# Kernel tuning notes

Measured on AMD Instinct MI355X. Metric: run time of the kernel, lower is better.

The kernel has to match this reference:

```python
import jax, jax.numpy as jnp
import numpy as np

EMBED_DIM = 1024
B, S = 4, 2048

def setup_inputs() -> dict:
    key = jax.random.key(0)
    ks = jax.random.split(key, 9)
    D = EMBED_DIM
    scale = 1.0 / np.sqrt(D)
    scale2 = 1.0 / np.sqrt(2 * D)
    return {
        "classical_state": jax.random.normal(ks[0], (B, S, D), jnp.float32),
        "quantum_state": jax.random.normal(ks[1], (B, S, D), jnp.float32),
        "Wc": jax.random.uniform(ks[2], (D, D), jnp.float32, -scale, scale),
        "bc": jax.random.uniform(ks[3], (D,), jnp.float32, -scale, scale),
        "Wq": jax.random.uniform(ks[4], (D, D), jnp.float32, -scale, scale),
        "bq": jax.random.uniform(ks[5], (D,), jnp.float32, -scale, scale),
        "Wg": jax.random.uniform(ks[6], (D, 2 * D), jnp.float32, -scale2, scale2),
        "bg": jax.random.uniform(ks[7], (D,), jnp.float32, -scale2, scale2),
        "temperature": jnp.array(1.0, jnp.float32),
    }

def reference(classical_state, quantum_state, Wc, bc, Wq, bq, Wg, bg, temperature):
    D = classical_state.shape[-1]
    c_proj = jnp.einsum('bsd,ed->bse', classical_state, Wc) + bc  # [B,S,D]
    q_proj = jnp.einsum('bsd,ed->bse', quantum_state, Wq) + bq    # [B,S,D]
    combined = jnp.concatenate([c_proj, q_proj], axis=-1)         # [B,S,2D]
    interface_state = jax.nn.sigmoid(jnp.einsum('bsf,ef->bse', combined, Wg) + bg)
    similarity = jnp.einsum('bsd,btd->bst', c_proj, q_proj) / jnp.sqrt(jnp.asarray(D, c_proj.dtype))
    attention_weights = jax.nn.softmax(similarity / temperature, axis=-1)  # [B,S,S]
    transfer_state = jnp.einsum('bst,btd->bsd', attention_weights, quantum_state)
    return classical_state + interface_state * transfer_state
```

## Files before the change

kernel.cpp:

```cpp
#include <hip/hip_runtime.h>


typedef unsigned short u16;
typedef unsigned char u8;
typedef __bf16 bf16x8 __attribute__((ext_vector_type(8)));
typedef float f32x4 __attribute__((ext_vector_type(4)));

__device__ __forceinline__ u16 f2bf(float f) {
    unsigned int x;
    __builtin_memcpy(&x, &f, 4);
    unsigned int r = x + 0x7FFFu + ((x >> 16) & 1u);
    return (u16)(r >> 16);
}
__device__ __forceinline__ float bf2f(u16 u) {
    unsigned int x = ((unsigned int)u) << 16;
    float f;
    __builtin_memcpy(&f, &x, 4);
    return f;
}
__device__ __forceinline__ u8 f2fp8(float f) {
    int p = __builtin_amdgcn_cvt_pk_fp8_f32(f, f, 0, false);
    return (u8)(p & 0xFF);
}

__device__ __forceinline__ void xcd_tile(int& tx, int& ty) {
    const int gx = gridDim.x;
    const int nwg = gx * gridDim.y;
    const int l = blockIdx.x + gx * blockIdx.y;
    const int per = nwg >> 3;
    const int swz = (l & 7) * per + (l >> 3);
    tx = swz % gx;
    ty = swz / gx;
}

#define GLOBAL_TO_LDS16(gp, lp)                                                           \
    __builtin_amdgcn_global_load_lds((const __attribute__((address_space(1))) void*)(gp), \
                                     (__attribute__((address_space(3))) void*)(lp), 16, 0, 0)

__global__ __launch_bounds__(256, 2) void gemm_proj(
    const u16* __restrict__ Ac, const u16* __restrict__ Aq, int lda,
    const u16* __restrict__ Bp, long sBz, int ldb,
    u8* __restrict__ C8, long sCz, int ldc, int K,
    const float* __restrict__ bc, const float* __restrict__ bq) {
    __shared__ __align__(16) u16 As[128 * 64];
    __shared__ __align__(16) u16 Bs[128 * 64];

    const int tid  = threadIdx.x;
    const int lane = tid & 63;
    const int wave = tid >> 6;
    const int z    = blockIdx.z;

    const u16* a = z ? Aq : Ac;
    const u16* b = Bp + (long)z * sBz;
    const float* bias = z ? bq : bc;

    int tx, ty;
    xcd_tile(tx, ty);
    const int tileM = ty * 128;
    const int tileN = tx * 128;

    const int wm  = wave >> 1;
    const int wn  = wave & 1;
    const int r16 = lane & 15;
    const int kg  = lane >> 4;

    const int srow = lane >> 3;
    const int sgc  = ((lane & 7) ^ (lane >> 3)) * 8;
    const int swb  = r16 & 7;

    f32x4 acc[4][4] = {};

    for (int k0 = 0; k0 < K; k0 += 64) {
#pragma unroll
        for (int p = 0; p < 4; p++) {
            const int rbase = p * 32 + wave * 8;
            GLOBAL_TO_LDS16(a + (long)(tileM + rbase + srow) * lda + k0 + sgc, &As[rbase * 64]);
            GLOBAL_TO_LDS16(b + (long)(tileN + rbase + srow) * ldb + k0 + sgc, &Bs[rbase * 64]);
        }
        __syncthreads();

        bf16x8 af[2][4], bfr[2][4];
#pragma unroll
        for (int h = 0; h < 2; h++) {
#pragma unroll
            for (int i = 0; i < 4; i++) {
                const int Ra = wm * 64 + i * 16 + r16;
                af[h][i]  = *(const bf16x8*)&As[Ra * 64 + (((h * 4 + kg) ^ swb)) * 8];
                const int Rb = wn * 64 + i * 16 + r16;
                bfr[h][i] = *(const bf16x8*)&Bs[Rb * 64 + (((h * 4 + kg) ^ swb)) * 8];
            }
        }
#pragma unroll
        for (int h = 0; h < 2; h++)
#pragma unroll
            for (int i = 0; i < 4; i++)
#pragma unroll
                for (int j = 0; j < 4; j++)
                    acc[i][j] = __builtin_amdgcn_mfma_f32_16x16x32_bf16(
                        af[h][i], bfr[h][j], acc[i][j], 0, 0, 0);
        __syncthreads();
    }

#pragma unroll
    for (int i = 0; i < 4; i++)
#pragma unroll
        for (int j = 0; j < 4; j++) {
            int col = tileN + wn * 64 + j * 16 + r16;
            float bv = bias[col];
#pragma unroll
            for (int v = 0; v < 4; v++) {
                int row = tileM + wm * 64 + i * 16 + kg * 4 + v;
                C8[(long)z * sCz + (long)row * ldc + col] = f2fp8(acc[i][j][v] + bv);
            }
        }
}

template <int MODE>
__global__ __launch_bounds__(256, 2) void gemm8(
    const u8* __restrict__ A0, const u8* __restrict__ A1, long sAz, int lda, int kSplit,
    const u8* __restrict__ Bp, long sBz, int ldb,
    void* __restrict__ Cp, long cOff, long sCz, int ldc, int K,
    const float* __restrict__ bias, const float* __restrict__ temp,
    const float* __restrict__ cls, const u16* __restrict__ g16,
    float* __restrict__ lsum, long lSz) {
    __shared__ __align__(16) u8 As[128 * 128];
    __shared__ __align__(16) u8 Bs[128 * 128];

    const int tid  = threadIdx.x;
    const int lane = tid & 63;
    const int wave = tid >> 6;
    const int z    = blockIdx.z;

    const u8* a = A0 + (long)z * sAz;
    const u8* b = Bp + (long)z * sBz;

    int tx, ty;
    xcd_tile(tx, ty);
    const int tileM = ty * 128;
    const int tileN = tx * 128;

    const int wm  = wave >> 1;
    const int wn  = wave & 1;
    const int r16 = lane & 15;
    const int kg  = lane >> 4;

    const int srow = lane >> 3;
    const int sgc  = ((lane & 7) ^ (lane >> 3)) * 16;

    f32x4 acc[4][4] = {};

    for (int k0 = 0; k0 < K; k0 += 128) {
        const u8* Ap = a;
        int kA = k0;
        if (MODE == 1 && k0 >= kSplit) { Ap = A1; kA = k0 - kSplit; }

#pragma unroll
        for (int p = 0; p < 4; p++) {
            const int rbase = p * 32 + wave * 8;
            GLOBAL_TO_LDS16(Ap + (long)(tileM + rbase + srow) * lda + kA + sgc, &As[rbase * 128]);
            GLOBAL_TO_LDS16(b + (long)(tileN + rbase + srow) * ldb + k0 + sgc, &Bs[rbase * 128]);
        }
        __syncthreads();

#pragma unroll
        for (int h = 0; h < 4; h++) {
            long af[4], bfr[4];
#pragma unroll
            for (int i = 0; i < 4; i++) {
                const int Ra = wm * 64 + i * 16 + r16;
                af[i]  = *(const long*)&As[Ra * 128 + (((h * 2 + (kg >> 1)) ^ (Ra & 7))) * 16 + (kg & 1) * 8];
                const int Rb = wn * 64 + i * 16 + r16;
                bfr[i] = *(const long*)&Bs[Rb * 128 + (((h * 2 + (kg >> 1)) ^ (Rb & 7))) * 16 + (kg & 1) * 8];
            }
#pragma unroll
            for (int i = 0; i < 4; i++)
#pragma unroll
                for (int j = 0; j < 4; j++)
                    acc[i][j] = __builtin_amdgcn_mfma_f32_16x16x32_fp8_fp8(
                        af[i], bfr[j], acc[i][j], 0, 0, 0);
        }
        __syncthreads();
    }

    float scale = 1.0f;
    if (MODE == 2) scale = 1.0f / (32.0f * temp[0]);

    u16*   C16 = (u16*)Cp;
    u8*    C8  = (u8*)Cp;
    float* C32 = (float*)Cp;

#pragma unroll
    for (int i = 0; i < 4; i++) {
        float rs[4] = {0.f, 0.f, 0.f, 0.f};
#pragma unroll
        for (int j = 0; j < 4; j++) {
            int col = tileN + wn * 64 + j * 16 + r16;
            float bv = (MODE == 1) ? bias[col] : 0.0f;
#pragma unroll
            for (int v = 0; v < 4; v++) {
                int row = tileM + wm * 64 + i * 16 + kg * 4 + v;
                long idx = cOff + (long)z * sCz + (long)row * ldc + col;
                float val = acc[i][j][v];
                if (MODE == 1) {
                    C16[idx] = f2bf(1.0f / (1.0f + __expf(-(val + bv))));
                } else if (MODE == 2) {
                    float e = __expf(val * scale);
                    C8[idx] = f2fp8(e);
                    rs[v] += e;
                } else {
                    float inv = 1.0f / lsum[(long)z * lSz + row];
                    C32[idx] = cls[idx] + bf2f(g16[idx]) * (val * inv);
                }
            }
        }
        if (MODE == 2) {
#pragma unroll
            for (int v = 0; v < 4; v++) {
                float s = rs[v];
#pragma unroll
                for (int off = 1; off < 16; off <<= 1) s += __shfl_xor(s, off, 64);
                if (r16 == 0) {
                    int row = tileM + wm * 64 + i * 16 + kg * 4 + v;
                    atomicAdd(&lsum[(long)z * lSz + row], s);
                }
            }
        }
    }
}

__global__ __launch_bounds__(256) void prep(
    const f32x4* __restrict__ cls, const f32x4* __restrict__ qnt,
    const f32x4* __restrict__ Wc, const f32x4* __restrict__ Wq, const f32x4* __restrict__ Wg,
    ushort4* __restrict__ clsB, ushort4* __restrict__ qntB,
    ushort4* __restrict__ WcB, ushort4* __restrict__ WqB, unsigned int* __restrict__ Wg8,
    f32x4* __restrict__ l, long nM, long nW, long nG, long nL) {
    long i = (long)blockIdx.x * 256 + threadIdx.x;
    long stride = (long)gridDim.x * 256;
    long total = 2 * nM + 2 * nW + nG + nL;
    for (; i < total; i += stride) {
        if (i < 2 * nM) {
            long j = (i < nM) ? i : i - nM;
            f32x4 v = (i < nM) ? cls[j] : qnt[j];
            ushort4 o;
            o.x = f2bf(v.x); o.y = f2bf(v.y); o.z = f2bf(v.z); o.w = f2bf(v.w);
            if (i < nM) clsB[j] = o; else qntB[j] = o;
        } else if (i < 2 * nM + 2 * nW) {
            long j = i - 2 * nM;
            long k = (j < nW) ? j : j - nW;
            f32x4 v = (j < nW) ? Wc[k] : Wq[k];
            ushort4 o;
            o.x = f2bf(v.x); o.y = f2bf(v.y); o.z = f2bf(v.z); o.w = f2bf(v.w);
            if (j < nW) WcB[k] = o; else WqB[k] = o;
        } else if (i < 2 * nM + 2 * nW + nG) {
            long j = i - 2 * nM - 2 * nW;
            f32x4 v = Wg[j];
            int w = __builtin_amdgcn_cvt_pk_fp8_f32(v.x, v.y, 0, false);
            w = __builtin_amdgcn_cvt_pk_fp8_f32(v.z, v.w, w, true);
            Wg8[j] = (unsigned int)w;
        } else {
            l[i - 2 * nM - 2 * nW - nG] = (f32x4){0.f, 0.f, 0.f, 0.f};
        }
    }
}

__global__ __launch_bounds__(256) void transpose_fp8(const u16* __restrict__ Q,
                                                     u8* __restrict__ QT, int S, int D) {
    __shared__ u8 tile[64][65];
    int bz = blockIdx.z;
    const u16* q = Q + (long)bz * S * D;
    u8* qt = QT + (long)bz * S * D;
    int t0 = blockIdx.x * 64;
    int d0 = blockIdx.y * 64;
    int c = threadIdx.x & 63;
    int r = threadIdx.x >> 6;
#pragma unroll
    for (int i = 0; i < 16; i++) {
        int tl = r + 4 * i;
        tile[tl][c] = f2fp8(bf2f(q[(long)(t0 + tl) * D + d0 + c]));
    }
    __syncthreads();
#pragma unroll
    for (int i = 0; i < 16; i++) {
        int dl = r + 4 * i;
        qt[(long)(d0 + dl) * S + t0 + c] = tile[c][dl];
    }
}

extern "C" void kernel_launch(void* const* d_in, const int* in_sizes, int n_in,
                              void* d_out, int out_size, void* d_ws, size_t ws_size,
                              hipStream_t stream) {
    (void)in_sizes; (void)n_in; (void)out_size;

    const float* classical = (const float*)d_in[0];
    const float* quantum   = (const float*)d_in[1];
    const float* Wc        = (const float*)d_in[2];
    const float* bc        = (const float*)d_in[3];
    const float* Wq        = (const float*)d_in[4];
    const float* bq        = (const float*)d_in[5];
    const float* Wg        = (const float*)d_in[6];
    const float* bg        = (const float*)d_in[7];
    const float* temp      = (const float*)d_in[8];
    float* out = (float*)d_out;

    const int B = 4, S = 2048, D = 1024;
    const long MD = (long)B * S * D;

    float* l    = (float*)d_ws;
    u16* Wc_b   = (u16*)(l + (long)B * S);
    u16* Wq_b   = Wc_b + (long)D * D;
    u8*  Wg8    = (u8*)(Wq_b + (long)D * D);
    u16* cls_b  = (u16*)(Wg8 + (long)D * 2 * D);
    u16* qnt_b  = cls_b + MD;
    u8*  cp8    = (u8*)(qnt_b + MD);
    u8*  qp8    = cp8 + MD;
    u8*  qT8    = qp8 + MD;
    u8*  P8     = qT8 + MD;
    u16* g      = cls_b;

    const size_t fixed_bytes = (size_t)B * S * 4 + 2 * (size_t)D * D * 2 +
        (size_t)D * 2 * D + 2 * (size_t)MD * 2 + 3 * (size_t)MD;
    int CH = 128;
    for (int c = 2048; c >= 128; c >>= 1) {
        if (ws_size >= fixed_bytes + (size_t)B * c * S) { CH = c; break; }
    }

    dim3 blk(256);

    prep<<<2048, blk, 0, stream>>>(
        (const f32x4*)classical, (const f32x4*)quantum,
        (const f32x4*)Wc, (const f32x4*)Wq, (const f32x4*)Wg,
        (ushort4*)cls_b, (ushort4*)qnt_b,
        (ushort4*)Wc_b, (ushort4*)Wq_b, (unsigned int*)Wg8,
        (f32x4*)l, MD / 4, (long)D * D / 4, (long)D * 2 * D / 4, (long)B * S / 4);

    gemm_proj<<<dim3(D / 128, (B * S) / 128, 2), blk, 0, stream>>>(
        cls_b, qnt_b, D, Wc_b, (long)D * D, D, cp8, MD, D, D, bc, bq);

    gemm8<1><<<dim3(D / 128, (B * S) / 128, 1), blk, 0, stream>>>(
        cp8, qp8, 0, D, D, Wg8, 0, 2 * D, g, 0, 0, D, 2 * D,
        bg, nullptr, nullptr, nullptr, nullptr, 0);

    transpose_fp8<<<dim3(S / 64, D / 64, B), blk, 0, stream>>>(qnt_b, qT8, S, D);

    for (int m0 = 0; m0 < S; m0 += CH) {
        gemm8<2><<<dim3(S / 128, CH / 128, B), blk, 0, stream>>>(
            cp8 + (long)m0 * D, nullptr, (long)S * D, D, 1 << 30,
            qp8, (long)S * D, D, P8, 0, (long)CH * S, S, D,
            nullptr, temp, nullptr, nullptr, l + m0, S);
        gemm8<4><<<dim3(D / 128, CH / 128, B), blk, 0, stream>>>(
            P8, nullptr, (long)CH * S, S, 1 << 30, qT8, (long)D * S, S,
            out, (long)m0 * D, (long)S * D, D, S,
            nullptr, nullptr, classical, g, l + m0, S);
    }
}
```

Measured before the change: 266.2 us.

## Double-buffer LDS tiles with async prefetch in projection and fp8 GEMMs

Both GEMM kernels now keep two LDS buffers for the A and B tiles and prefetch the tile two k-steps ahead with global_load_lds. They use explicit vmcnt waits and raw s_barrier in place of __syncthreads. The aim is to overlap global-to-LDS loads with MFMA compute instead of stalling on each tile load. This doubles LDS use, to 64 KB per block, which may limit occupancy under launch_bounds(256,2), and it depends on the vmcnt count matching the 8 loads issued per stage.

```diff
diff --git a/kernel.cpp b/kernel.cpp
--- a/kernel.cpp
+++ b/kernel.cpp
@@ -42,8 +42,8 @@
     const u16* __restrict__ Bp, long sBz, int ldb,
     u8* __restrict__ C8, long sCz, int ldc, int K,
     const float* __restrict__ bc, const float* __restrict__ bq) {
-    __shared__ __align__(16) u16 As[128 * 64];
-    __shared__ __align__(16) u16 Bs[128 * 64];
+    __shared__ __align__(16) u16 As[2][128 * 64];
+    __shared__ __align__(16) u16 Bs[2][128 * 64];
 
     const int tid  = threadIdx.x;
     const int lane = tid & 63;
@@ -68,16 +68,28 @@
     const int sgc  = ((lane & 7) ^ (lane >> 3)) * 8;
     const int swb  = r16 & 7;
 
-    f32x4 acc[4][4] = {};
-
-    for (int k0 = 0; k0 < K; k0 += 64) {
+    auto stage = [&](int buf, int t) {
+        const int k0 = t * 64;
 #pragma unroll
         for (int p = 0; p < 4; p++) {
             const int rbase = p * 32 + wave * 8;
-            GLOBAL_TO_LDS16(a + (long)(tileM + rbase + srow) * lda + k0 + sgc, &As[rbase * 64]);
-            GLOBAL_TO_LDS16(b + (long)(tileN + rbase + srow) * ldb + k0 + sgc, &Bs[rbase * 64]);
-        }
-        __syncthreads();
+            GLOBAL_TO_LDS16(a + (long)(tileM + rbase + srow) * lda + k0 + sgc, &As[buf][rbase * 64]);
+            GLOBAL_TO_LDS16(b + (long)(tileN + rbase + srow) * ldb + k0 + sgc, &Bs[buf][rbase * 64]);
+        }
+    };
+
+    f32x4 acc[4][4] = {};
+
+    const int nt = K / 64;
+    stage(0, 0);
+    stage(1, 1);
+
+    for (int t = 0; t < nt; t++) {
+        const int cur = t & 1;
+        if (t + 1 < nt) asm volatile("s_waitcnt vmcnt(8)" ::: "memory");
+        else            asm volatile("s_waitcnt vmcnt(0)" ::: "memory");
+        __builtin_amdgcn_s_barrier();
+        asm volatile("" ::: "memory");
 
         bf16x8 af[2][4], bfr[2][4];
 #pragma unroll
@@ -85,9 +97,9 @@
 #pragma unroll
             for (int i = 0; i < 4; i++) {
                 const int Ra = wm * 64 + i * 16 + r16;
-                af[h][i]  = *(const bf16x8*)&As[Ra * 64 + (((h * 4 + kg) ^ swb)) * 8];
+                af[h][i]  = *(const bf16x8*)&As[cur][Ra * 64 + (((h * 4 + kg) ^ swb)) * 8];
                 const int Rb = wn * 64 + i * 16 + r16;
-                bfr[h][i] = *(const bf16x8*)&Bs[Rb * 64 + (((h * 4 + kg) ^ swb)) * 8];
+                bfr[h][i] = *(const bf16x8*)&Bs[cur][Rb * 64 + (((h * 4 + kg) ^ swb)) * 8];
             }
         }
 #pragma unroll
@@ -98,7 +110,10 @@
                 for (int j = 0; j < 4; j++)
                     acc[i][j] = __builtin_amdgcn_mfma_f32_16x16x32_bf16(
                         af[h][i], bfr[h][j], acc[i][j], 0, 0, 0);
-        __syncthreads();
+
+        asm volatile("" ::: "memory");
+        __builtin_amdgcn_s_barrier();
+        if (t + 2 < nt) stage(cur, t + 2);
     }
 
 #pragma unroll
@@ -123,8 +138,8 @@
     const float* __restrict__ bias, const float* __restrict__ temp,
     const float* __restrict__ cls, const u16* __restrict__ g16,
     float* __restrict__ lsum, long lSz) {
-    __shared__ __align__(16) u8 As[128 * 128];
-    __shared__ __align__(16) u8 Bs[128 * 128];
+    __shared__ __align__(16) u8 As[2][128 * 128];
+    __shared__ __align__(16) u8 Bs[2][128 * 128];
 
     const int tid  = threadIdx.x;
     const int lane = tid & 63;
@@ -147,20 +162,31 @@
     const int srow = lane >> 3;
     const int sgc  = ((lane & 7) ^ (lane >> 3)) * 16;
 
-    f32x4 acc[4][4] = {};
-
-    for (int k0 = 0; k0 < K; k0 += 128) {
+    auto stage = [&](int buf, int t) {
+        const int k0 = t * 128;
         const u8* Ap = a;
         int kA = k0;
         if (MODE == 1 && k0 >= kSplit) { Ap = A1; kA = k0 - kSplit; }
-
 #pragma unroll
         for (int p = 0; p < 4; p++) {
             const int rbase = p * 32 + wave * 8;
-            GLOBAL_TO_LDS16(Ap + (long)(tileM + rbase + srow) * lda + kA + sgc, &As[rbase * 128]);
-            GLOBAL_TO_LDS16(b + (long)(tileN + rbase + srow) * ldb + k0 + sgc, &Bs[rbase * 128]);
-        }
-        __syncthreads();
+            GLOBAL_TO_LDS16(Ap + (long)(tileM + rbase + srow) * lda + kA + sgc, &As[buf][rbase * 128]);
+            GLOBAL_TO_LDS16(b + (long)(tileN + rbase + srow) * ldb + k0 + sgc, &Bs[buf][rbase * 128]);
+        }
+    };
+
+    f32x4 acc[4][4] = {};
+
+    const int nt = K / 128;
+    stage(0, 0);
+    stage(1, 1);
+
+    for (int t = 0; t < nt; t++) {
+        const int cur = t & 1;
+        if (t + 1 < nt) asm volatile("s_waitcnt vmcnt(8)" ::: "memory");
+        else            asm volatile("s_waitcnt vmcnt(0)" ::: "memory");
+        __builtin_amdgcn_s_barrier();
+        asm volatile("" ::: "memory");
 
 #pragma unroll
         for (int h = 0; h < 4; h++) {
@@ -168,9 +194,9 @@
 #pragma unroll
             for (int i = 0; i < 4; i++) {
                 const int Ra = wm * 64 + i * 16 + r16;
-                af[i]  = *(const long*)&As[Ra * 128 + (((h * 2 + (kg >> 1)) ^ (Ra & 7))) * 16 + (kg & 1) * 8];
+                af[i]  = *(const long*)&As[cur][Ra * 128 + (((h * 2 + (kg >> 1)) ^ (Ra & 7))) * 16 + (kg & 1) * 8];
                 const int Rb = wn * 64 + i * 16 + r16;
-                bfr[i] = *(const long*)&Bs[Rb * 128 + (((h * 2 + (kg >> 1)) ^ (Rb & 7))) * 16 + (kg & 1) * 8];
+                bfr[i] = *(const long*)&Bs[cur][Rb * 128 + (((h * 2 + (kg >> 1)) ^ (Rb & 7))) * 16 + (kg & 1) * 8];
             }
 #pragma unroll
             for (int i = 0; i < 4; i++)
@@ -179,7 +205,10 @@
                     acc[i][j] = __builtin_amdgcn_mfma_f32_16x16x32_fp8_fp8(
                         af[i], bfr[j], acc[i][j], 0, 0, 0);
         }
-        __syncthreads();
+
+        asm volatile("" ::: "memory");
+        __builtin_amdgcn_s_barrier();
+        if (t + 2 < nt) stage(cur, t + 2);
     }
 
     float scale = 1.0f;
```

Measured after the change: 281.5 us. 5.8% more time.
